# Optimization experiments

Measured on AMD Instinct MI355X. Metric: run time of the kernel, lower is better.

The kernel has to match this reference:

```python
import math
import jax, jax.numpy as jnp
import numpy as np

B, L, D = 2, 2048, 1024
NH = 16
HS = D // NH
BLOCK_SIZE = 2048


def setup_inputs() -> dict:
    key = jax.random.key(0)
    ks = jax.random.split(key, 4)
    x = jax.random.normal(ks[0], (B, L, D), dtype=jnp.float32)
    Wqkv = jax.random.normal(ks[1], (D, 3 * D), dtype=jnp.float32) * 0.02
    bqkv = jnp.zeros((3 * D,), dtype=jnp.float32)
    Wproj = jax.random.normal(ks[2], (D, D), dtype=jnp.float32) * 0.02
    bproj = jnp.zeros((D,), dtype=jnp.float32)
    Er = jax.random.normal(ks[3], (BLOCK_SIZE, HS), dtype=jnp.float32)
    return {"x": x, "Wqkv": Wqkv, "bqkv": bqkv, "Wproj": Wproj, "bproj": bproj, "Er": Er}


def _skew(QEr):
    # QEr: [B, nh, L, L]  (Music Transformer skew trick)
    b, nh, nr, nc = QEr.shape
    padded = jnp.pad(QEr, ((0, 0), (0, 0), (0, 0), (1, 0)))  # [B, nh, nr, nc+1]
    reshaped = padded.reshape(b, nh, nc + 1, nr)
    return reshaped[:, :, 1:, :]  # [B, nh, nr, nc]


def reference(x, Wqkv, bqkv, Wproj, bproj, Er):
    b, l, d = x.shape
    qkv = x @ Wqkv + bqkv  # [B, L, 3D]
    q, k, v = jnp.split(qkv, 3, axis=2)
    q = q.reshape(b, l, NH, HS).transpose(0, 2, 1, 3)  # [B, nh, L, hs]
    k = k.reshape(b, l, NH, HS).transpose(0, 2, 1, 3)
    v = v.reshape(b, l, NH, HS).transpose(0, 2, 1, 3)

    start = BLOCK_SIZE - l
    Er_t = Er[start:, :].T  # [hs, L]
    QEr = jnp.einsum('bhld,dm->bhlm', q, Er_t)  # [B, nh, L, L]
    Srel = _skew(QEr)

    QK_t = jnp.einsum('bhld,bhmd->bhlm', q, k)
    scale = 1.0 / math.sqrt(HS)
    att = (QK_t + Srel) * scale
    causal = jnp.tril(jnp.ones((l, l), dtype=bool))
    att = jnp.where(causal[None, None, :, :], att, jnp.float32(-jnp.inf))
    att = jax.nn.softmax(att, axis=-1)
    y = jnp.einsum('bhlm,bhmd->bhld', att, v)
    y = y.transpose(0, 2, 1, 3).reshape(b, l, d)
    return y @ Wproj + bproj
```

## Files before the change

### kernel.cpp

```cpp
#include <hip/hip_runtime.h>
#include <stdint.h>

#define BB 2
#define LL 2048
#define DD 1024
#define NHH 16
#define HSS 64

typedef __bf16 bf16x8 __attribute__((ext_vector_type(8)));
typedef float f32x4 __attribute__((ext_vector_type(4)));

__device__ __forceinline__ bf16x8 load8(const float* p) {
  float4 f0 = *(const float4*)p;
  float4 f1 = *(const float4*)(p + 4);
  bf16x8 v;
  v[0] = (__bf16)f0.x; v[1] = (__bf16)f0.y; v[2] = (__bf16)f0.z; v[3] = (__bf16)f0.w;
  v[4] = (__bf16)f1.x; v[5] = (__bf16)f1.y; v[6] = (__bf16)f1.z; v[7] = (__bf16)f1.w;
  return v;
}
__device__ __forceinline__ bf16x8 load8(const __bf16* p) {
  return *(const bf16x8*)p;
}

__device__ __forceinline__ void async_ld16(__bf16* lds_uniform_base,
                                           const __bf16* gptr_per_lane) {
  __builtin_amdgcn_global_load_lds(
      (const __attribute__((address_space(1))) void*)gptr_per_lane,
      (__attribute__((address_space(3))) void*)lds_uniform_base, 16, 0, 0);
}

__global__ void prep_k(const float* __restrict__ Wqkv, const float* __restrict__ x,
                       const float* __restrict__ Er, __bf16* __restrict__ WqkvT,
                       __bf16* __restrict__ xb, __bf16* __restrict__ Erb) {
  int tx = threadIdx.x, ty = threadIdx.y;
  int tid = ty * 32 + tx;
  if (blockIdx.z == 1) {
    if (blockIdx.x >= 2048) return;
    size_t off = ((size_t)blockIdx.x * 256 + tid) * 8;
    *(bf16x8*)&xb[off] = load8(&x[off]);
    return;
  }
  if (blockIdx.z == 2) {
    if (blockIdx.x >= 64) return;
    size_t off = ((size_t)blockIdx.x * 256 + tid) * 8;
    *(bf16x8*)&Erb[off] = load8(&Er[off]);
    return;
  }
  __shared__ __bf16 tile[32][33];
  int c0 = (blockIdx.x % 96) * 32, r0 = (blockIdx.x / 96) * 32;
#pragma unroll
  for (int i = ty; i < 32; i += 8)
    tile[i][tx] = (__bf16)Wqkv[(size_t)(r0 + i) * 3072 + c0 + tx];
  __syncthreads();
#pragma unroll
  for (int i = ty; i < 32; i += 8)
    WqkvT[(size_t)(c0 + i) * 1024 + r0 + tx] = tile[tx][i];
}

__global__ __launch_bounds__(256) void gemm_qkv_k(
    const __bf16* __restrict__ A, const __bf16* __restrict__ Bt,
    const float* __restrict__ bias, __bf16* __restrict__ Qo,
    __bf16* __restrict__ Ko, __bf16* __restrict__ Vto) {
  const int K = 1024;
  __shared__ __align__(16) __bf16 As[128 * 32];
  __shared__ __align__(16) __bf16 Bs[128 * 32];
  __shared__ __align__(16) __bf16 Vl[64 * 136];
  int t = threadIdx.x;
  int wave = t >> 6, lane = t & 63, qd = lane >> 4, lr = lane & 15;
  int m0 = blockIdx.y * 128, n0 = blockIdx.x * 128;
  int wm = (wave >> 1) * 64, wn = (wave & 1) * 64;
  f32x4 acc[4][4] = {};
  int srow = lane >> 2, sch = (lane & 3) * 8;
  const __bf16* Ab[2];
  const __bf16* Bb[2];
#pragma unroll
  for (int c = 0; c < 2; c++) {
    Ab[c] = A + (size_t)(m0 + (wave * 2 + c) * 16 + srow) * K + sch;
    Bb[c] = Bt + (size_t)(n0 + (wave * 2 + c) * 16 + srow) * K + sch;
  }
  for (int k0 = 0; k0 < K; k0 += 32) {
    __syncthreads();
#pragma unroll
    for (int c = 0; c < 2; c++) {
      async_ld16(&As[(wave * 2 + c) * 512], Ab[c] + k0);
      async_ld16(&Bs[(wave * 2 + c) * 512], Bb[c] + k0);
    }
    __syncthreads();
    bf16x8 af[4], bfr[4];
#pragma unroll
    for (int mt = 0; mt < 4; mt++)
      af[mt] = *(const bf16x8*)&As[(wm + mt * 16 + lr) * 32 + qd * 8];
#pragma unroll
    for (int nt = 0; nt < 4; nt++)
      bfr[nt] = *(const bf16x8*)&Bs[(wn + nt * 16 + lr) * 32 + qd * 8];
#pragma unroll
    for (int mt = 0; mt < 4; mt++)
#pragma unroll
      for (int nt = 0; nt < 4; nt++)
        acc[mt][nt] = __builtin_amdgcn_mfma_f32_16x16x32_bf16(af[mt], bfr[nt],
                                                              acc[mt][nt], 0, 0, 0);
  }
  float bvv[4];
#pragma unroll
  for (int nt = 0; nt < 4; nt++) bvv[nt] = bias[n0 + wn + nt * 16 + lr];

  if (n0 < 2 * DD) {
#pragma unroll
    for (int mt = 0; mt < 4; mt++)
#pragma unroll
      for (int nt = 0; nt < 4; nt++)
#pragma unroll
        for (int r = 0; r < 4; r++) {
          int row = m0 + wm + mt * 16 + qd * 4 + r;
          int col = n0 + wn + nt * 16 + lr;
          __bf16 bb = (__bf16)(acc[mt][nt][r] + bvv[nt]);
          int b = row >> 11, l = row & 2047;
          int h = (col >> 6) & 15, d = col & 63;
          if (col < DD) {
            Qo[(((size_t)(b * NHH + h)) * LL + l) * HSS + d] = bb;
          } else {
            Ko[(((size_t)(b * NHH + h)) * LL + l) * HSS + d] = bb;
          }
        }
  } else {
    int vb0 = n0 - 2 * DD;
    int bq = m0 >> 11, l0 = m0 & 2047;
    int vr = t >> 2, vc = (t & 3) * 8;
#pragma unroll
    for (int c = 0; c < 2; c++) {
      if ((wave & 1) == c) {
#pragma unroll
        for (int mt = 0; mt < 4; mt++)
#pragma unroll
          for (int nt = 0; nt < 4; nt++)
#pragma unroll
            for (int r = 0; r < 4; r++) {
              int vrow = nt * 16 + lr;
              int ml = wm + mt * 16 + qd * 4 + r;
              Vl[vrow * 136 + ml] = (__bf16)(acc[mt][nt][r] + bvv[nt]);
            }
      }
      __syncthreads();
      int h = (vb0 + c * 64) >> 6;
      __bf16* dst = Vto + (((size_t)(bq * NHH + h)) * HSS + vr) * LL + l0 + vc;
      const __bf16* src = &Vl[vr * 136 + vc];
#pragma unroll
      for (int u = 0; u < 4; u++)
        *(bf16x8*)(dst + u * 32) = *(const bf16x8*)(src + u * 32);
      __syncthreads();
    }
  }
}

__global__ __launch_bounds__(256) void gemm_proj_k(
    const __bf16* __restrict__ A, const __bf16* __restrict__ Bt,
    const float* __restrict__ bias, float* __restrict__ out) {
  const int K = 1024, N = 1024;
  __shared__ __align__(16) __bf16 As[128 * 32];
  __shared__ __align__(16) __bf16 Bs[64 * 32];
  int t = threadIdx.x;
  int wave = t >> 6, lane = t & 63, qd = lane >> 4, lr = lane & 15;
  int m0 = blockIdx.y * 128, n0 = blockIdx.x * 64;
  int wm = (wave >> 1) * 64, wn = (wave & 1) * 32;
  f32x4 acc[4][2] = {};
  int srow = lane >> 2, sch = (lane & 3) * 8;
  const __bf16* Ab[2];
  const __bf16* Bb;
#pragma unroll
  for (int c = 0; c < 2; c++)
    Ab[c] = A + (size_t)(m0 + (wave * 2 + c) * 16 + srow) * K + sch;
  Bb = Bt + (size_t)(n0 + wave * 16 + srow) * K + sch;

  for (int k0 = 0; k0 < K; k0 += 32) {
    __syncthreads();
#pragma unroll
    for (int c = 0; c < 2; c++)
      async_ld16(&As[(wave * 2 + c) * 512], Ab[c] + k0);
    async_ld16(&Bs[wave * 512], Bb + k0);
    __syncthreads();
    bf16x8 af[4], bfr[2];
#pragma unroll
    for (int mt = 0; mt < 4; mt++)
      af[mt] = *(const bf16x8*)&As[(wm + mt * 16 + lr) * 32 + qd * 8];
#pragma unroll
    for (int nt = 0; nt < 2; nt++)
      bfr[nt] = *(const bf16x8*)&Bs[(wn + nt * 16 + lr) * 32 + qd * 8];
#pragma unroll
    for (int mt = 0; mt < 4; mt++)
#pragma unroll
      for (int nt = 0; nt < 2; nt++)
        acc[mt][nt] = __builtin_amdgcn_mfma_f32_16x16x32_bf16(af[mt], bfr[nt],
                                                              acc[mt][nt], 0, 0, 0);
  }
  float bvv[2];
#pragma unroll
  for (int nt = 0; nt < 2; nt++) bvv[nt] = bias[n0 + wn + nt * 16 + lr];
#pragma unroll
  for (int mt = 0; mt < 4; mt++)
#pragma unroll
    for (int nt = 0; nt < 2; nt++)
#pragma unroll
      for (int r = 0; r < 4; r++) {
        int row = m0 + wm + mt * 16 + qd * 4 + r;
        int col = n0 + wn + nt * 16 + lr;
        out[(size_t)row * N + col] = acc[mt][nt][r] + bvv[nt];
      }
}

__global__ __launch_bounds__(256, 3) void flash_k(
    const __bf16* __restrict__ Qg, const __bf16* __restrict__ Kg,
    const __bf16* __restrict__ Vtg, const __bf16* __restrict__ Erb,
    __bf16* __restrict__ Po0, __bf16* __restrict__ Po1,
    float* __restrict__ Lp0, float* __restrict__ Lp1) {
  __shared__ __align__(16) __bf16 Kbuf[2][64 * 64];
  __shared__ __align__(16) __bf16 Vbuf[2][64 * 64];
  __shared__ __align__(16) __bf16 Pball[4][16 * 64];

  int bh = blockIdx.x;
  int tile = 31 - (int)blockIdx.y;
  int i0 = tile * 64;
  int niter = tile + 1;
  int mid = (niter + 1) >> 1;
  int it0 = (blockIdx.z == 0) ? 0 : mid;
  int it1 = (blockIdx.z == 0) ? mid : niter;
  const __bf16* Qh = Qg + (size_t)bh * LL * HSS;
  const __bf16* Kh = Kg + (size_t)bh * LL * HSS;
  const __bf16* Vth = Vtg + (size_t)bh * HSS * LL;
  int b = bh >> 4, h = bh & 15;
  int t = threadIdx.x, wave = t >> 6, lane = t & 63, qd = lane >> 4, lr = lane & 15;
  __bf16* Pb = &Pball[wave][0];
  int cbase = 48 - wave * 16;

  const float SC = 0.18033688011112042f;

  int lrow = lane >> 3;
  int lcol = ((lane & 7) ^ lrow) * 8;
  const __bf16* KsrcB[2];
  const __bf16* VsrcB[2];
#pragma unroll
  for (int c = 0; c < 2; c++) {
    int q = wave * 2 + c;
    KsrcB[c] = Kh + (size_t)(q * 8 + lrow) * HSS + lcol;
    VsrcB[c] = Vth + (size_t)(q * 8 + lrow) * LL + lcol;
  }

  int swA = (qd ^ (lr & 7)) * 8;
  int swB = ((qd + 4) ^ (lr & 7)) * 8;

  int hi8 = lr >> 3;
  int ib0 = 15 - qd * 4 + lr;
  int pb0 = qd * 256 + (lr & 7);
  int px0 = (qd & 1) * 4;
  int rowb = i0 + wave * 16 + qd * 4;

  bf16x8 aq[2];
  {
    const __bf16* qrow = Qh + (size_t)(i0 + wave * 16 + lr) * HSS + qd * 8;
    aq[0] = *(const bf16x8*)qrow;
    aq[1] = *(const bf16x8*)(qrow + 32);
  }
  f32x4 oacc[4] = {};
  float lsum[4] = {};

  int cur = 0;
  if (it0 < it1) {
    int j0 = it0 * 64;
#pragma unroll
    for (int c = 0; c < 2; c++) {
      async_ld16(&Kbuf[0][(wave * 2 + c) * 512], KsrcB[c] + (size_t)j0 * HSS);
      async_ld16(&Vbuf[0][(wave * 2 + c) * 512], VsrcB[c] + j0);
    }
  }
  __syncthreads();

  for (int it = it0; it < it1; ++it) {
    int j0 = it * 64;

    if (it + 1 < it1) {
      int jn = (it + 1) * 64;
#pragma unroll
      for (int c = 0; c < 2; c++) {
        async_ld16(&Kbuf[cur ^ 1][(wave * 2 + c) * 512], KsrcB[c] + (size_t)jn * HSS);
        async_ld16(&Vbuf[cur ^ 1][(wave * 2 + c) * 512], VsrcB[c] + jn);
      }
    }

    int ebase = LL - 64 - i0 + j0 + cbase + lr;
    int e[5];
#pragma unroll
    for (int ct = 0; ct < 5; ct++) {
      int v = ebase + ct * 16;
      e[ct] = (v < LL) ? v : (LL - 1);
    }
    bf16x8 ef0[5];
#pragma unroll
    for (int ct = 0; ct < 5; ct++)
      ef0[ct] = *(const bf16x8*)&Erb[(size_t)e[ct] * HSS + qd * 8];

    const __bf16* Kb = &Kbuf[cur][0];
    const __bf16* Vb = &Vbuf[cur][0];

    f32x4 sacc[4] = {};
    __builtin_amdgcn_s_setprio(1);
#pragma unroll
    for (int ct = 0; ct < 4; ct++) {
      bf16x8 bk0 = *(const bf16x8*)&Kb[(ct * 16 + lr) * 64 + swA];
      bf16x8 bk1 = *(const bf16x8*)&Kb[(ct * 16 + lr) * 64 + swB];
      sacc[ct] = __builtin_amdgcn_mfma_f32_16x16x32_bf16(aq[0], bk0, sacc[ct], 0, 0, 0);
      sacc[ct] = __builtin_amdgcn_mfma_f32_16x16x32_bf16(aq[1], bk1, sacc[ct], 0, 0, 0);
    }
    __builtin_amdgcn_s_setprio(0);

    bf16x8 ef1[5];
#pragma unroll
    for (int ct = 0; ct < 5; ct++)
      ef1[ct] = *(const bf16x8*)&Erb[(size_t)e[ct] * HSS + 32 + qd * 8];

    f32x4 racc[5] = {};
    __builtin_amdgcn_s_setprio(1);
#pragma unroll
    for (int ct = 0; ct < 5; ct++)
      racc[ct] = __builtin_amdgcn_mfma_f32_16x16x32_bf16(aq[0], ef0[ct], racc[ct], 0, 0, 0);
#pragma unroll
    for (int ct = 0; ct < 5; ct++)
      racc[ct] = __builtin_amdgcn_mfma_f32_16x16x32_bf16(aq[1], ef1[ct], racc[ct], 0, 0, 0);
    __builtin_amdgcn_s_setprio(0);

    int dib = rowb - j0;
#pragma unroll
    for (int r = 0; r < 4; r++) {
      int bse = ib0 - r;
      int hi = bse >> 4;
      int idx = (qd * 16 + (bse & 15)) << 2;
      float sh[5];
#pragma unroll
      for (int ct = 0; ct < 5; ct++)
        sh[ct] = __int_as_float(
            __builtin_amdgcn_ds_bpermute(idx, __float_as_int(racc[ct][r])));
      int di = dib + r;
#pragma unroll
      for (int ct2 = 0; ct2 < 4; ct2++) {
        float rel = hi ? sh[ct2 + 1] : sh[ct2];
        float p = __builtin_exp2f((sacc[ct2][r] + rel) * SC);
        p = (ct2 * 16 + lr <= di) ? p : 0.f;
        __bf16 pb = (__bf16)p;
        lsum[r] += (float)pb;
        Pb[pb0 + r * 64 + (((2 * ct2 + hi8) ^ (px0 + r)) << 3)] = pb;
      }
    }

    bf16x8 ap0 = *(const bf16x8*)&Pb[lr * 64 + swA];
    bf16x8 ap1 = *(const bf16x8*)&Pb[lr * 64 + swB];
    __builtin_amdgcn_s_setprio(1);
#pragma unroll
    for (int dt = 0; dt < 4; dt++) {
      bf16x8 bv0 = *(const bf16x8*)&Vb[(dt * 16 + lr) * 64 + swA];
      bf16x8 bv1 = *(const bf16x8*)&Vb[(dt * 16 + lr) * 64 + swB];
      oacc[dt] = __builtin_amdgcn_mfma_f32_16x16x32_bf16(ap0, bv0, oacc[dt], 0, 0, 0);
      oacc[dt] = __builtin_amdgcn_mfma_f32_16x16x32_bf16(ap1, bv1, oacc[dt], 0, 0, 0);
    }
    __builtin_amdgcn_s_setprio(0);

    __syncthreads();
    cur ^= 1;
  }

#pragma unroll
  for (int r = 0; r < 4; r++) {
#pragma unroll
    for (int m = 1; m < 16; m <<= 1)
      lsum[r] += __shfl_xor(lsum[r], m, 64);
  }

  __bf16* Po = (blockIdx.z == 0) ? Po0 : Po1;
  float* Lp = (blockIdx.z == 0) ? Lp0 : Lp1;
#pragma unroll
  for (int r = 0; r < 4; r++) {
    int l = i0 + wave * 16 + qd * 4 + r;
    if (lr == 0) Lp[(size_t)bh * LL + l] = lsum[r];
#pragma unroll
    for (int dt = 0; dt < 4; dt++) {
      int d = dt * 16 + lr;
      Po[((size_t)(b * LL) + l) * DD + h * HSS + d] = (__bf16)oacc[dt][r];
    }
  }
}

__global__ void ct_k(const __bf16* __restrict__ Po0,
                     const __bf16* __restrict__ Po1,
                     const float* __restrict__ Lp0,
                     const float* __restrict__ Lp1,
                     __bf16* __restrict__ Y,
                     const float* __restrict__ Wproj,
                     __bf16* __restrict__ WprojT) {
  int id = blockIdx.x;
  if (id < 2048) {
    size_t f = ((size_t)id * 256 + threadIdx.x) * 8;
    int dfull = (int)(f & 1023);
    int h = dfull >> 6;
    int l = (int)((f >> 10) & 2047);
    int b = (int)(f >> 21);
    size_t lidx = ((size_t)(b * NHH + h)) * LL + l;
    float linv = 1.f / (Lp0[lidx] + Lp1[lidx]);
    bf16x8 a = *(const bf16x8*)&Po0[f];
    bf16x8 c = *(const bf16x8*)&Po1[f];
    bf16x8 o;
#pragma unroll
    for (int q = 0; q < 8; q++)
      o[q] = (__bf16)(((float)a[q] + (float)c[q]) * linv);
    *(bf16x8*)&Y[f] = o;
    return;
  }
  __shared__ __bf16 tile[32][33];
  int q = id - 2048;
  int c0 = (q & 31) * 32, r0 = (q >> 5) * 32;
  int tx = threadIdx.x & 31, ty = threadIdx.x >> 5;
#pragma unroll
  for (int i = ty; i < 32; i += 8)
    tile[i][tx] = (__bf16)Wproj[(size_t)(r0 + i) * 1024 + c0 + tx];
  __syncthreads();
#pragma unroll
  for (int i = ty; i < 32; i += 8)
    WprojT[(size_t)(c0 + i) * 1024 + r0 + tx] = tile[tx][i];
}

extern "C" void kernel_launch(void* const* d_in, const int* in_sizes, int n_in,
                              void* d_out, int out_size, void* d_ws, size_t ws_size,
                              hipStream_t stream) {
  const float* x = (const float*)d_in[0];
  const float* Wqkv = (const float*)d_in[1];
  const float* bqkv = (const float*)d_in[2];
  const float* Wproj = (const float*)d_in[3];
  const float* bproj = (const float*)d_in[4];
  const float* Er = (const float*)d_in[5];
  float* out = (float*)d_out;

  if (ws_size < 4u * 8388608u) return;

  uint8_t* w = (uint8_t*)d_ws;
  __bf16* Q = (__bf16*)w;  w += (size_t)BB * NHH * LL * HSS * 2;
  __bf16* Kt = (__bf16*)w; w += (size_t)BB * NHH * LL * HSS * 2;
  __bf16* Vt = (__bf16*)w; w += (size_t)BB * NHH * LL * HSS * 2;
  __bf16* Y = (__bf16*)w;  w += (size_t)BB * LL * DD * 2;

  __bf16* WqkvT = (__bf16*)d_out;
  __bf16* xb = (__bf16*)((uint8_t*)d_out + (size_t)3072 * 1024 * 2);
  __bf16* Erb = (__bf16*)((uint8_t*)d_out + (size_t)3072 * 1024 * 2 + (size_t)4096 * 1024 * 2);
  __bf16* Po1 = (__bf16*)d_out;
  float* Lp0 = (float*)((uint8_t*)d_out + (size_t)BB * LL * DD * 2);
  float* Lp1 = (float*)((uint8_t*)d_out + (size_t)BB * LL * DD * 2 + (size_t)BB * NHH * LL * 4);
  __bf16* Po0 = Y;
  __bf16* WprojT = Q;

  prep_k<<<dim3(3072, 1, 3), dim3(32, 8), 0, stream>>>(Wqkv, x, Er, WqkvT, xb, Erb);
  gemm_qkv_k<<<dim3(3072 / 128, 4096 / 128), 256, 0, stream>>>(
      xb, WqkvT, bqkv, Q, Kt, Vt);
  flash_k<<<dim3(BB * NHH, 32, 2), 256, 0, stream>>>(
      Q, Kt, Vt, Erb, Po0, Po1, Lp0, Lp1);
  ct_k<<<dim3(3072), 256, 0, stream>>>(Po0, Po1, Lp0, Lp1, Y, Wproj, WprojT);
  gemm_proj_k<<<dim3(1024 / 64, 4096 / 128), 256, 0, stream>>>(Y, WprojT, bproj, out);
}
```

Before: 241.5 us.

## Compute softmax row sums via MFMA with ones vector and batch bpermutes

Replaces the per-element scalar accumulation of probability row sums (and the final cross-lane shuffle reduction) with two extra MFMAs that multiply the P tile by a ones column, giving row sums in an extra accumulator. It also hoists all Er loads to the top of the iteration and issues all bpermutes before the exponent loop to improve latency hiding. This adds MFMA work and register pressure (extra accumulator, 20 live shuffled values, 10 Er vectors) in exchange for fewer VALU ops.

```diff
diff --git a/kernel.cpp b/kernel.cpp
--- a/kernel.cpp
+++ b/kernel.cpp
@@ -233,6 +233,10 @@
 
   const float SC = 0.18033688011112042f;
 
+  bf16x8 bones;
+#pragma unroll
+  for (int q = 0; q < 8; q++) bones[q] = (lr == 0) ? (__bf16)1.f : (__bf16)0.f;
+
   int lrow = lane >> 3;
   int lcol = ((lane & 7) ^ lrow) * 8;
   const __bf16* KsrcB[2];
@@ -259,8 +263,7 @@
     aq[0] = *(const bf16x8*)qrow;
     aq[1] = *(const bf16x8*)(qrow + 32);
   }
-  f32x4 oacc[4] = {};
-  float lsum[4] = {};
+  f32x4 oacc[5] = {};
 
   int cur = 0;
   if (it0 < it1) {
@@ -286,16 +289,14 @@
     }
 
     int ebase = LL - 64 - i0 + j0 + cbase + lr;
-    int e[5];
+    bf16x8 ef0[5], ef1[5];
 #pragma unroll
     for (int ct = 0; ct < 5; ct++) {
       int v = ebase + ct * 16;
-      e[ct] = (v < LL) ? v : (LL - 1);
-    }
-    bf16x8 ef0[5];
-#pragma unroll
-    for (int ct = 0; ct < 5; ct++)
-      ef0[ct] = *(const bf16x8*)&Erb[(size_t)e[ct] * HSS + qd * 8];
+      int e = (v < LL) ? v : (LL - 1);
+      ef0[ct] = *(const bf16x8*)&Erb[(size_t)e * HSS + qd * 8];
+      ef1[ct] = *(const bf16x8*)&Erb[(size_t)e * HSS + 32 + qd * 8];
+    }
 
     const __bf16* Kb = &Kbuf[cur][0];
     const __bf16* Vb = &Vbuf[cur][0];
@@ -311,11 +312,6 @@
     }
     __builtin_amdgcn_s_setprio(0);
 
-    bf16x8 ef1[5];
-#pragma unroll
-    for (int ct = 0; ct < 5; ct++)
-      ef1[ct] = *(const bf16x8*)&Erb[(size_t)e[ct] * HSS + 32 + qd * 8];
-
     f32x4 racc[5] = {};
     __builtin_amdgcn_s_setprio(1);
 #pragma unroll
@@ -326,26 +322,27 @@
       racc[ct] = __builtin_amdgcn_mfma_f32_16x16x32_bf16(aq[1], ef1[ct], racc[ct], 0, 0, 0);
     __builtin_amdgcn_s_setprio(0);
 
+    float sh[4][5];
+#pragma unroll
+    for (int r = 0; r < 4; r++) {
+      int idx = (qd * 16 + ((ib0 - r) & 15)) << 2;
+#pragma unroll
+      for (int ct = 0; ct < 5; ct++)
+        sh[r][ct] = __int_as_float(
+            __builtin_amdgcn_ds_bpermute(idx, __float_as_int(racc[ct][r])));
+    }
+
     int dib = rowb - j0;
 #pragma unroll
     for (int r = 0; r < 4; r++) {
-      int bse = ib0 - r;
-      int hi = bse >> 4;
-      int idx = (qd * 16 + (bse & 15)) << 2;
-      float sh[5];
-#pragma unroll
-      for (int ct = 0; ct < 5; ct++)
-        sh[ct] = __int_as_float(
-            __builtin_amdgcn_ds_bpermute(idx, __float_as_int(racc[ct][r])));
+      int hi = (ib0 - r) >> 4;
       int di = dib + r;
 #pragma unroll
       for (int ct2 = 0; ct2 < 4; ct2++) {
-        float rel = hi ? sh[ct2 + 1] : sh[ct2];
+        float rel = hi ? sh[r][ct2 + 1] : sh[r][ct2];
         float p = __builtin_exp2f((sacc[ct2][r] + rel) * SC);
         p = (ct2 * 16 + lr <= di) ? p : 0.f;
-        __bf16 pb = (__bf16)p;
-        lsum[r] += (float)pb;
-        Pb[pb0 + r * 64 + (((2 * ct2 + hi8) ^ (px0 + r)) << 3)] = pb;
+        Pb[pb0 + r * 64 + (((2 * ct2 + hi8) ^ (px0 + r)) << 3)] = (__bf16)p;
       }
     }
 
@@ -359,25 +356,20 @@
       oacc[dt] = __builtin_amdgcn_mfma_f32_16x16x32_bf16(ap0, bv0, oacc[dt], 0, 0, 0);
       oacc[dt] = __builtin_amdgcn_mfma_f32_16x16x32_bf16(ap1, bv1, oacc[dt], 0, 0, 0);
     }
+    oacc[4] = __builtin_amdgcn_mfma_f32_16x16x32_bf16(ap0, bones, oacc[4], 0, 0, 0);
+    oacc[4] = __builtin_amdgcn_mfma_f32_16x16x32_bf16(ap1, bones, oacc[4], 0, 0, 0);
     __builtin_amdgcn_s_setprio(0);
 
     __syncthreads();
     cur ^= 1;
   }
 
-#pragma unroll
-  for (int r = 0; r < 4; r++) {
-#pragma unroll
-    for (int m = 1; m < 16; m <<= 1)
-      lsum[r] += __shfl_xor(lsum[r], m, 64);
-  }
-
   __bf16* Po = (blockIdx.z == 0) ? Po0 : Po1;
   float* Lp = (blockIdx.z == 0) ? Lp0 : Lp1;
 #pragma unroll
   for (int r = 0; r < 4; r++) {
     int l = i0 + wave * 16 + qd * 4 + r;
-    if (lr == 0) Lp[(size_t)bh * LL + l] = lsum[r];
+    if (lr == 0) Lp[(size_t)bh * LL + l] = oacc[4][r];
 #pragma unroll
     for (int dt = 0; dt < 4; dt++) {
       int d = dt * 16 + lr;
```

Result: no change. 245.0 us (+1.5%).
